# Kernel tuning notes

Measured on AMD Instinct MI355X. Metric: run time of the kernel, lower is better.

## Reference

```python
import jax, jax.numpy as jnp
import numpy as np

Q_BITS = 4
Q_MAX = 2 ** (Q_BITS - 1) - 1  # 7 for 4-bit symmetric

B, S, D_IN, D_OUT = 4, 2048, 4096, 11008


def setup_inputs() -> dict:
    key = jax.random.key(0)
    kx, kw = jax.random.split(key)
    x = jax.random.normal(kx, (B, S, D_IN), dtype=jnp.float32)
    weight = jax.random.normal(kw, (D_OUT, D_IN), dtype=jnp.float32)
    bias = jnp.zeros((1, D_OUT), dtype=jnp.float32)
    return {"x": x, "weight": weight, "bias": bias}


def _quant_act_per_token_absmax(t):
    # t: [N, D]; symmetric fake-quant with per-token (per-row) absmax scale
    scales = jnp.max(jnp.abs(t), axis=-1, keepdims=True)
    scales = jnp.maximum(scales, 1e-5) / Q_MAX
    return jnp.round(t / scales) * scales


def reference(x, weight, bias):
    x_shape = x.shape
    xf = x.reshape(-1, x_shape[-1])          # [B*S, D_in]
    q_x = _quant_act_per_token_absmax(xf)    # fake-quantized activations
    y = q_x @ weight.T + bias                # [B*S, D_out]
    return y.reshape(x_shape[0], x_shape[1], -1)
```

## Files before the change

kernel.cpp:

```cpp
#include <hip/hip_runtime.h>
#include <hip/hip_bf16.h>

#define M_DIM 8192
#define N_DIM 11008
#define K_DIM 4096
#define NT 32
#define RROW ((size_t)64 * K_DIM)

typedef __attribute__((ext_vector_type(4))) int i32x4;

__global__ void quant_x_kernel(const float* __restrict__ x,
                               char* __restrict__ xq, float* __restrict__ sx) {
  const int row = blockIdx.x;
  const int t = threadIdx.x;
  const float4* xr4 = (const float4*)(x + (size_t)row * K_DIM);
  float4 v[4];
  float amax = 0.0f;
#pragma unroll
  for (int i = 0; i < 4; ++i) {
    v[i] = xr4[t + 256 * i];
    amax = fmaxf(amax, fmaxf(fmaxf(fabsf(v[i].x), fabsf(v[i].y)),
                             fmaxf(fabsf(v[i].z), fabsf(v[i].w))));
  }
#pragma unroll
  for (int off = 32; off > 0; off >>= 1)
    amax = fmaxf(amax, __shfl_xor(amax, off, 64));
  __shared__ float red[4];
  if ((t & 63) == 0) red[t >> 6] = amax;
  __syncthreads();
  amax = fmaxf(fmaxf(red[0], red[1]), fmaxf(red[2], red[3]));
  const float s = fmaxf(amax, 1e-5f) / 7.0f;
  if (t == 0) sx[row] = s;
  char q[16];
#pragma unroll
  for (int i = 0; i < 4; ++i) {
    q[i * 4 + 0] = (char)(int)rintf(v[i].x / s);
    q[i * 4 + 1] = (char)(int)rintf(v[i].y / s);
    q[i * 4 + 2] = (char)(int)rintf(v[i].z / s);
    q[i * 4 + 3] = (char)(int)rintf(v[i].w / s);
  }
  *(int4*)(xq + (size_t)row * K_DIM + t * 16) = *(int4*)q;
}

__global__ void quant_w_kernel(const float* __restrict__ w,
                               char* __restrict__ wq, float* __restrict__ sw) {
  const int row = blockIdx.x;
  const int t = threadIdx.x;
  const float4* wr4 = (const float4*)(w + (size_t)row * K_DIM);
  float4 v[4];
  float amax = 0.0f;
#pragma unroll
  for (int i = 0; i < 4; ++i) {
    v[i] = wr4[t + 256 * i];
    amax = fmaxf(amax, fmaxf(fmaxf(fabsf(v[i].x), fabsf(v[i].y)),
                             fmaxf(fabsf(v[i].z), fabsf(v[i].w))));
  }
#pragma unroll
  for (int off = 32; off > 0; off >>= 1)
    amax = fmaxf(amax, __shfl_xor(amax, off, 64));
  __shared__ float red[4];
  if ((t & 63) == 0) red[t >> 6] = amax;
  __syncthreads();
  amax = fmaxf(fmaxf(red[0], red[1]), fmaxf(red[2], red[3]));
  const float s = fmaxf(amax, 1e-30f) / 127.0f;
  if (t == 0) sw[row] = s;
  char q[16];
#pragma unroll
  for (int i = 0; i < 4; ++i) {
    q[i * 4 + 0] = (char)(int)rintf(v[i].x / s);
    q[i * 4 + 1] = (char)(int)rintf(v[i].y / s);
    q[i * 4 + 2] = (char)(int)rintf(v[i].z / s);
    q[i * 4 + 3] = (char)(int)rintf(v[i].w / s);
  }
  *(int4*)(wq + (size_t)row * K_DIM + t * 16) = *(int4*)q;
}

#define GL(g, d)                                                             \
  __builtin_amdgcn_global_load_lds(                                          \
      (const __attribute__((address_space(1))) void*)(g),                    \
      (__attribute__((address_space(3))) void*)(d), 16, 0, 0)

template<bool STG>
__device__ __forceinline__ void tile_body(const char* paRow, const char* pbRow, int colswz,
    const char* gAn, const char* gBn, char* dA, char* dB, i32x4 (&acc)[8][4]) {
  if constexpr (STG) {
    GL(gAn, dA);                    GL(gAn + 2 * RROW, dA + 16384);
    GL(gBn, dB);                    GL(gBn + RROW, dB + 8192);
    GL(gBn + 2 * RROW, dB + 16384); GL(gBn + 3 * RROW, dB + 24576);
    GL(gAn + RROW, dA + 8192);      GL(gAn + 3 * RROW, dA + 24576);
  }
  const int c0 = colswz;
  const int c1 = colswz ^ 64;
  i32x4 a0[4], a1[4], a2[4], a3[4], b0[4], b1[4];
#pragma unroll
  for (int i = 0; i < 4; ++i) a0[i] = *(const i32x4*)(paRow + i * 2048 + c0);
#pragma unroll
  for (int i = 0; i < 4; ++i) b0[i] = *(const i32x4*)(pbRow + i * 2048 + c0);
#pragma unroll
  for (int i = 0; i < 4; ++i) a1[i] = *(const i32x4*)(paRow + 8192 + i * 2048 + c0);
#pragma unroll
  for (int m = 0; m < 4; ++m)
#pragma unroll
    for (int n = 0; n < 4; ++n)
      acc[m][n] = __builtin_amdgcn_mfma_i32_16x16x64_i8(a0[m], b0[n], acc[m][n], 0, 0, 0);
#pragma unroll
  for (int i = 0; i < 4; ++i) a2[i] = *(const i32x4*)(paRow + i * 2048 + c1);
#pragma unroll
  for (int i = 0; i < 4; ++i) b1[i] = *(const i32x4*)(pbRow + i * 2048 + c1);
#pragma unroll
  for (int m = 0; m < 4; ++m)
#pragma unroll
    for (int n = 0; n < 4; ++n)
      acc[4 + m][n] = __builtin_amdgcn_mfma_i32_16x16x64_i8(a1[m], b0[n], acc[4 + m][n], 0, 0, 0);
#pragma unroll
  for (int i = 0; i < 4; ++i) a3[i] = *(const i32x4*)(paRow + 8192 + i * 2048 + c1);
#pragma unroll
  for (int m = 0; m < 4; ++m)
#pragma unroll
    for (int n = 0; n < 4; ++n)
      acc[m][n] = __builtin_amdgcn_mfma_i32_16x16x64_i8(a2[m], b1[n], acc[m][n], 0, 0, 0);
#pragma unroll
  for (int m = 0; m < 4; ++m)
#pragma unroll
    for (int n = 0; n < 4; ++n)
      acc[4 + m][n] = __builtin_amdgcn_mfma_i32_16x16x64_i8(a3[m], b1[n], acc[4 + m][n], 0, 0, 0);
}

__global__ __launch_bounds__(512, 2) void gemm_kernel(
    const char* __restrict__ xq, const char* __restrict__ wq,
    const float* __restrict__ sx, const float* __restrict__ sw,
    const float* __restrict__ bias, float* __restrict__ out) {
  __shared__ char lds_c[131072];

  const int tid = threadIdx.x;
  const int lane = tid & 63;
  const int wave = tid >> 6;
  const int wm = wave >> 2;
  const int wn = wave & 3;
  const int lr = lane & 15;

  const int bid = blockIdx.x;
  const int sw_id = (bid & 7) * 172 + (bid >> 3);
  const int bm = sw_id / 43, bn = sw_id % 43;
  const int m0 = bm * 256, n0 = bn * 256;

  const int srow = tid >> 3;
  const int srccb = ((tid & 7) << 4) ^ ((srow & 7) << 4);
  const char* gA0 = xq + (size_t)(m0 + srow) * K_DIM + srccb;
  const char* gB0 = wq + (size_t)(n0 + srow) * K_DIM + srccb;
  char* dA0 = lds_c + wave * 1024;
  char* dB0 = lds_c + 65536 + wave * 1024;

  const int aRowOff = (wm * 128 + lr) * 128;
  const int bRowOff = (wn * 64 + lr) * 128;
  const int colswz = ((lane >> 4) << 4) ^ ((lr & 7) << 4);

  i32x4 acc[8][4] = {};

  GL(gA0, dA0);                    GL(gA0 + 2 * RROW, dA0 + 16384);
  GL(gB0, dB0);                    GL(gB0 + RROW, dB0 + 8192);
  GL(gB0 + 2 * RROW, dB0 + 16384); GL(gB0 + 3 * RROW, dB0 + 24576);
  GL(gA0 + RROW, dA0 + 8192);      GL(gA0 + 3 * RROW, dA0 + 24576);
  __syncthreads();

  for (int t = 0; t < NT - 1; ++t) {
    const int buf = t & 1;
    tile_body<true>(lds_c + buf * 32768 + aRowOff,
                    lds_c + 65536 + buf * 32768 + bRowOff, colswz,
                    gA0 + (size_t)(t + 1) * 128, gB0 + (size_t)(t + 1) * 128,
                    dA0 + (1 - buf) * 32768, dB0 + (1 - buf) * 32768, acc);
    __syncthreads();
  }
  tile_body<false>(lds_c + ((NT - 1) & 1) * 32768 + aRowOff,
                   lds_c + 65536 + ((NT - 1) & 1) * 32768 + bRowOff, colswz,
                   nullptr, nullptr, nullptr, nullptr, acc);

  const int orow0 = m0 + wm * 128 + (lane >> 4) * 4;
  const int ocol0 = n0 + wn * 64 + lr;
  float bv[4], swv[4];
#pragma unroll
  for (int fc = 0; fc < 4; ++fc) {
    bv[fc] = bias[ocol0 + fc * 16];
    swv[fc] = sw[ocol0 + fc * 16];
  }
#pragma unroll
  for (int fr = 0; fr < 8; ++fr) {
#pragma unroll
    for (int j = 0; j < 4; ++j) {
      const int grow = orow0 + fr * 16 + j;
      const float s = sx[grow];
      float* op = out + (size_t)grow * N_DIM + ocol0;
#pragma unroll
      for (int fc = 0; fc < 4; ++fc)
        op[fc * 16] = (float)acc[fr][fc][j] * (s * swv[fc]) + bv[fc];
    }
  }
}

extern "C" void kernel_launch(void* const* d_in, const int* in_sizes, int n_in,
                              void* d_out, int out_size, void* d_ws, size_t ws_size,
                              hipStream_t stream) {
  (void)in_sizes; (void)n_in; (void)out_size; (void)ws_size;
  const float* x = (const float*)d_in[0];
  const float* w = (const float*)d_in[1];
  const float* bias = (const float*)d_in[2];
  float* out = (float*)d_out;

  char* ws = (char*)d_ws;
  float* sx = (float*)ws;
  float* sw = (float*)(ws + 32768);
  char* xq8 = ws + 131072;
  char* wq8 = ws + 131072 + (size_t)M_DIM * K_DIM;

  quant_x_kernel<<<M_DIM, 256, 0, stream>>>(x, xq8, sx);
  quant_w_kernel<<<N_DIM, 256, 0, stream>>>(w, wq8, sw);
  gemm_kernel<<<dim3((M_DIM / 256) * (N_DIM / 256)), 512, 0, stream>>>(xq8, wq8, sx, sw, bias, out);
}
```

Measured before the change: 452.2 us.

## Software-pipeline MFMA groups across K tiles with sched barriers

Restructures the GEMM main loop so the last MFMA group of each K tile is deferred into the next tile. There it overlaps with the LDS reads issued after the barrier, and the barrier moves to the start of each tile. Sched barriers pin the interleaving of LDS reads and MFMA groups, so matrix work is always pending while fragments load. This costs extra registers for the carried fragments, which may pressure occupancy at 2 blocks of 512 threads.

```diff
diff --git a/kernel.cpp b/kernel.cpp
--- a/kernel.cpp
+++ b/kernel.cpp
@@ -80,50 +80,56 @@
       (const __attribute__((address_space(1))) void*)(g),                    \
       (__attribute__((address_space(3))) void*)(d), 16, 0, 0)
 
-template<bool STG>
-__device__ __forceinline__ void tile_body(const char* paRow, const char* pbRow, int colswz,
-    const char* gAn, const char* gBn, char* dA, char* dB, i32x4 (&acc)[8][4]) {
+template<int KK>
+__device__ __forceinline__ void read_g1(const char* paRow, const char* pbRow, int colswz,
+                                        i32x4 (&a)[4], i32x4 (&b)[4]) {
+  const int c = colswz ^ (KK * 64);
+#pragma unroll
+  for (int i = 0; i < 4; ++i) a[i] = *(const i32x4*)(paRow + i * 2048 + c);
+#pragma unroll
+  for (int i = 0; i < 4; ++i) b[i] = *(const i32x4*)(pbRow + i * 2048 + c);
+}
+template<int KK>
+__device__ __forceinline__ void read_g2(const char* paRow, int colswz, i32x4 (&a)[4]) {
+  const int c = colswz ^ (KK * 64);
+#pragma unroll
+  for (int i = 0; i < 4; ++i) a[i] = *(const i32x4*)(paRow + 8192 + i * 2048 + c);
+}
+template<int OFF>
+__device__ __forceinline__ void mfma16(const i32x4 (&a)[4], const i32x4 (&b)[4],
+                                       i32x4 (&acc)[8][4]) {
+#pragma unroll
+  for (int m = 0; m < 4; ++m)
+#pragma unroll
+    for (int n = 0; n < 4; ++n)
+      acc[OFF + m][n] = __builtin_amdgcn_mfma_i32_16x16x64_i8(a[m], b[n], acc[OFF + m][n], 0, 0, 0);
+}
+
+template<bool FIRST, bool STG>
+__device__ __forceinline__ void tile(const char* paRow, const char* pbRow, int colswz,
+    const char* gAn, const char* gBn, char* dA, char* dB,
+    i32x4 (&acc)[8][4], i32x4 (&bP)[4], i32x4 (&a2P)[4]) {
+  __syncthreads();
   if constexpr (STG) {
     GL(gAn, dA);                    GL(gAn + 2 * RROW, dA + 16384);
     GL(gBn, dB);                    GL(gBn + RROW, dB + 8192);
     GL(gBn + 2 * RROW, dB + 16384); GL(gBn + 3 * RROW, dB + 24576);
     GL(gAn + RROW, dA + 8192);      GL(gAn + 3 * RROW, dA + 24576);
   }
-  const int c0 = colswz;
-  const int c1 = colswz ^ 64;
-  i32x4 a0[4], a1[4], a2[4], a3[4], b0[4], b1[4];
-#pragma unroll
-  for (int i = 0; i < 4; ++i) a0[i] = *(const i32x4*)(paRow + i * 2048 + c0);
-#pragma unroll
-  for (int i = 0; i < 4; ++i) b0[i] = *(const i32x4*)(pbRow + i * 2048 + c0);
-#pragma unroll
-  for (int i = 0; i < 4; ++i) a1[i] = *(const i32x4*)(paRow + 8192 + i * 2048 + c0);
-#pragma unroll
-  for (int m = 0; m < 4; ++m)
-#pragma unroll
-    for (int n = 0; n < 4; ++n)
-      acc[m][n] = __builtin_amdgcn_mfma_i32_16x16x64_i8(a0[m], b0[n], acc[m][n], 0, 0, 0);
-#pragma unroll
-  for (int i = 0; i < 4; ++i) a2[i] = *(const i32x4*)(paRow + i * 2048 + c1);
-#pragma unroll
-  for (int i = 0; i < 4; ++i) b1[i] = *(const i32x4*)(pbRow + i * 2048 + c1);
-#pragma unroll
-  for (int m = 0; m < 4; ++m)
-#pragma unroll
-    for (int n = 0; n < 4; ++n)
-      acc[4 + m][n] = __builtin_amdgcn_mfma_i32_16x16x64_i8(a1[m], b0[n], acc[4 + m][n], 0, 0, 0);
-#pragma unroll
-  for (int i = 0; i < 4; ++i) a3[i] = *(const i32x4*)(paRow + 8192 + i * 2048 + c1);
-#pragma unroll
-  for (int m = 0; m < 4; ++m)
-#pragma unroll
-    for (int n = 0; n < 4; ++n)
-      acc[m][n] = __builtin_amdgcn_mfma_i32_16x16x64_i8(a2[m], b1[n], acc[m][n], 0, 0, 0);
-#pragma unroll
-  for (int m = 0; m < 4; ++m)
-#pragma unroll
-    for (int n = 0; n < 4; ++n)
-      acc[4 + m][n] = __builtin_amdgcn_mfma_i32_16x16x64_i8(a3[m], b1[n], acc[4 + m][n], 0, 0, 0);
+  i32x4 a10[4], b0[4], a20[4], a11[4], b1[4], a21[4];
+  read_g1<0>(paRow, pbRow, colswz, a10, b0);
+  if constexpr (!FIRST) mfma16<4>(a2P, bP, acc);
+  __builtin_amdgcn_sched_barrier(0);
+  read_g2<0>(paRow, colswz, a20);
+  mfma16<0>(a10, b0, acc);
+  __builtin_amdgcn_sched_barrier(0);
+  read_g1<1>(paRow, pbRow, colswz, a11, b1);
+  mfma16<4>(a20, b0, acc);
+  __builtin_amdgcn_sched_barrier(0);
+  read_g2<1>(paRow, colswz, a21);
+  mfma16<0>(a11, b1, acc);
+#pragma unroll
+  for (int i = 0; i < 4; ++i) { bP[i] = b1[i]; a2P[i] = a21[i]; }
 }
 
 __global__ __launch_bounds__(512, 2) void gemm_kernel(
@@ -156,24 +162,26 @@
   const int colswz = ((lane >> 4) << 4) ^ ((lr & 7) << 4);
 
   i32x4 acc[8][4] = {};
+  i32x4 bP[4], a2P[4];
 
   GL(gA0, dA0);                    GL(gA0 + 2 * RROW, dA0 + 16384);
   GL(gB0, dB0);                    GL(gB0 + RROW, dB0 + 8192);
   GL(gB0 + 2 * RROW, dB0 + 16384); GL(gB0 + 3 * RROW, dB0 + 24576);
   GL(gA0 + RROW, dA0 + 8192);      GL(gA0 + 3 * RROW, dA0 + 24576);
-  __syncthreads();
-
-  for (int t = 0; t < NT - 1; ++t) {
+
+  tile<true, true>(lds_c + aRowOff, lds_c + 65536 + bRowOff, colswz,
+                   gA0 + 128, gB0 + 128, dA0 + 32768, dB0 + 32768, acc, bP, a2P);
+  for (int t = 1; t < NT - 1; ++t) {
     const int buf = t & 1;
-    tile_body<true>(lds_c + buf * 32768 + aRowOff,
-                    lds_c + 65536 + buf * 32768 + bRowOff, colswz,
-                    gA0 + (size_t)(t + 1) * 128, gB0 + (size_t)(t + 1) * 128,
-                    dA0 + (1 - buf) * 32768, dB0 + (1 - buf) * 32768, acc);
-    __syncthreads();
-  }
-  tile_body<false>(lds_c + ((NT - 1) & 1) * 32768 + aRowOff,
-                   lds_c + 65536 + ((NT - 1) & 1) * 32768 + bRowOff, colswz,
-                   nullptr, nullptr, nullptr, nullptr, acc);
+    tile<false, true>(lds_c + buf * 32768 + aRowOff,
+                      lds_c + 65536 + buf * 32768 + bRowOff, colswz,
+                      gA0 + (size_t)(t + 1) * 128, gB0 + (size_t)(t + 1) * 128,
+                      dA0 + (1 - buf) * 32768, dB0 + (1 - buf) * 32768, acc, bP, a2P);
+  }
+  tile<false, false>(lds_c + ((NT - 1) & 1) * 32768 + aRowOff,
+                     lds_c + 65536 + ((NT - 1) & 1) * 32768 + bRowOff, colswz,
+                     nullptr, nullptr, nullptr, nullptr, acc, bP, a2P);
+  mfma16<4>(a2P, bP, acc);
 
   const int orow0 = m0 + wm * 128 + (lane >> 4) * 4;
   const int ocol0 = n0 + wn * 64 + lr;
```

New measurement: 436.3 us. -3.5%, faster.

## Load B fragments directly from global into registers, stage only A in LDS

Applied to the files above, without the earlier changes.

The GEMM no longer stages the weight tile through LDS. Each wave loads its B fragments straight from global memory into registers, prefetching the next half-K slice during the MFMA work, while A stays double-buffered in LDS. This halves LDS usage and removes B's LDS write/read traffic, and the block index mapping changes to a column-major tile order. In exchange each B row is fetched once per wave (wm duplicates) instead of once per block, and the code depends on register prefetch latency hiding; N=11008 is not a multiple of 256, so the bn tail handling should be checked.

```diff
diff --git a/kernel.cpp b/kernel.cpp
--- a/kernel.cpp
+++ b/kernel.cpp
@@ -80,57 +80,50 @@
       (const __attribute__((address_space(1))) void*)(g),                    \
       (__attribute__((address_space(3))) void*)(d), 16, 0, 0)
 
-template<bool STG>
-__device__ __forceinline__ void tile_body(const char* paRow, const char* pbRow, int colswz,
-    const char* gAn, const char* gBn, char* dA, char* dB, i32x4 (&acc)[8][4]) {
+#define MFMA_I8 __builtin_amdgcn_mfma_i32_16x16x64_i8
+
+template<bool STG, bool PB>
+__device__ __forceinline__ void tile(const char* pa, int colswz,
+    const char* gAn, char* dA, const char* gBt,
+    i32x4 (&bk0)[4], i32x4 (&bk1)[4], i32x4 (&acc)[8][4]) {
+  __syncthreads();
   if constexpr (STG) {
-    GL(gAn, dA);                    GL(gAn + 2 * RROW, dA + 16384);
-    GL(gBn, dB);                    GL(gBn + RROW, dB + 8192);
-    GL(gBn + 2 * RROW, dB + 16384); GL(gBn + 3 * RROW, dB + 24576);
-    GL(gAn + RROW, dA + 8192);      GL(gAn + 3 * RROW, dA + 24576);
-  }
-  const int c0 = colswz;
-  const int c1 = colswz ^ 64;
-  i32x4 a0[4], a1[4], a2[4], a3[4], b0[4], b1[4];
-#pragma unroll
-  for (int i = 0; i < 4; ++i) a0[i] = *(const i32x4*)(paRow + i * 2048 + c0);
-#pragma unroll
-  for (int i = 0; i < 4; ++i) b0[i] = *(const i32x4*)(pbRow + i * 2048 + c0);
-#pragma unroll
-  for (int i = 0; i < 4; ++i) a1[i] = *(const i32x4*)(paRow + 8192 + i * 2048 + c0);
-#pragma unroll
-  for (int m = 0; m < 4; ++m)
+    GL(gAn, dA);                GL(gAn + RROW, dA + 8192);
+    GL(gAn + 2 * RROW, dA + 16384); GL(gAn + 3 * RROW, dA + 24576);
+  }
+#pragma unroll
+  for (int f = 0; f < 4; ++f)
+    bk1[f] = *(const i32x4*)(gBt + 64 + (size_t)f * 16 * K_DIM);
+  i32x4 a[8];
+#pragma unroll
+  for (int f = 0; f < 8; ++f)
+    a[f] = *(const i32x4*)(pa + f * 2048 + colswz);
+#pragma unroll
+  for (int m = 0; m < 8; ++m)
 #pragma unroll
     for (int n = 0; n < 4; ++n)
-      acc[m][n] = __builtin_amdgcn_mfma_i32_16x16x64_i8(a0[m], b0[n], acc[m][n], 0, 0, 0);
-#pragma unroll
-  for (int i = 0; i < 4; ++i) a2[i] = *(const i32x4*)(paRow + i * 2048 + c1);
-#pragma unroll
-  for (int i = 0; i < 4; ++i) b1[i] = *(const i32x4*)(pbRow + i * 2048 + c1);
-#pragma unroll
-  for (int m = 0; m < 4; ++m)
+      acc[m][n] = MFMA_I8(a[m], bk0[n], acc[m][n], 0, 0, 0);
+  __builtin_amdgcn_sched_barrier(0);
+  if constexpr (PB) {
+#pragma unroll
+    for (int f = 0; f < 4; ++f)
+      bk0[f] = *(const i32x4*)(gBt + 128 + (size_t)f * 16 * K_DIM);
+  }
+#pragma unroll
+  for (int f = 0; f < 8; ++f)
+    a[f] = *(const i32x4*)(pa + f * 2048 + (colswz ^ 64));
+#pragma unroll
+  for (int m = 0; m < 8; ++m)
 #pragma unroll
     for (int n = 0; n < 4; ++n)
-      acc[4 + m][n] = __builtin_amdgcn_mfma_i32_16x16x64_i8(a1[m], b0[n], acc[4 + m][n], 0, 0, 0);
-#pragma unroll
-  for (int i = 0; i < 4; ++i) a3[i] = *(const i32x4*)(paRow + 8192 + i * 2048 + c1);
-#pragma unroll
-  for (int m = 0; m < 4; ++m)
-#pragma unroll
-    for (int n = 0; n < 4; ++n)
-      acc[m][n] = __builtin_amdgcn_mfma_i32_16x16x64_i8(a2[m], b1[n], acc[m][n], 0, 0, 0);
-#pragma unroll
-  for (int m = 0; m < 4; ++m)
-#pragma unroll
-    for (int n = 0; n < 4; ++n)
-      acc[4 + m][n] = __builtin_amdgcn_mfma_i32_16x16x64_i8(a3[m], b1[n], acc[4 + m][n], 0, 0, 0);
+      acc[m][n] = MFMA_I8(a[m], bk1[n], acc[m][n], 0, 0, 0);
 }
 
 __global__ __launch_bounds__(512, 2) void gemm_kernel(
     const char* __restrict__ xq, const char* __restrict__ wq,
     const float* __restrict__ sx, const float* __restrict__ sw,
     const float* __restrict__ bias, float* __restrict__ out) {
-  __shared__ char lds_c[131072];
+  __shared__ char lds_c[65536];
 
   const int tid = threadIdx.x;
   const int lane = tid & 63;
@@ -141,39 +134,36 @@
 
   const int bid = blockIdx.x;
   const int sw_id = (bid & 7) * 172 + (bid >> 3);
-  const int bm = sw_id / 43, bn = sw_id % 43;
+  const int bm = sw_id & 31, bn = sw_id >> 5;
   const int m0 = bm * 256, n0 = bn * 256;
 
   const int srow = tid >> 3;
   const int srccb = ((tid & 7) << 4) ^ ((srow & 7) << 4);
   const char* gA0 = xq + (size_t)(m0 + srow) * K_DIM + srccb;
-  const char* gB0 = wq + (size_t)(n0 + srow) * K_DIM + srccb;
   char* dA0 = lds_c + wave * 1024;
-  char* dB0 = lds_c + 65536 + wave * 1024;
 
   const int aRowOff = (wm * 128 + lr) * 128;
-  const int bRowOff = (wn * 64 + lr) * 128;
   const int colswz = ((lane >> 4) << 4) ^ ((lr & 7) << 4);
 
+  const char* gB0 = wq + (size_t)(n0 + wn * 64 + lr) * K_DIM + ((lane >> 4) << 4);
+
   i32x4 acc[8][4] = {};
-
-  GL(gA0, dA0);                    GL(gA0 + 2 * RROW, dA0 + 16384);
-  GL(gB0, dB0);                    GL(gB0 + RROW, dB0 + 8192);
-  GL(gB0 + 2 * RROW, dB0 + 16384); GL(gB0 + 3 * RROW, dB0 + 24576);
-  GL(gA0 + RROW, dA0 + 8192);      GL(gA0 + 3 * RROW, dA0 + 24576);
-  __syncthreads();
+  i32x4 bk0[4], bk1[4];
+
+  GL(gA0, dA0);                GL(gA0 + RROW, dA0 + 8192);
+  GL(gA0 + 2 * RROW, dA0 + 16384); GL(gA0 + 3 * RROW, dA0 + 24576);
+#pragma unroll
+  for (int f = 0; f < 4; ++f)
+    bk0[f] = *(const i32x4*)(gB0 + (size_t)f * 16 * K_DIM);
 
   for (int t = 0; t < NT - 1; ++t) {
     const int buf = t & 1;
-    tile_body<true>(lds_c + buf * 32768 + aRowOff,
-                    lds_c + 65536 + buf * 32768 + bRowOff, colswz,
-                    gA0 + (size_t)(t + 1) * 128, gB0 + (size_t)(t + 1) * 128,
-                    dA0 + (1 - buf) * 32768, dB0 + (1 - buf) * 32768, acc);
-    __syncthreads();
-  }
-  tile_body<false>(lds_c + ((NT - 1) & 1) * 32768 + aRowOff,
-                   lds_c + 65536 + ((NT - 1) & 1) * 32768 + bRowOff, colswz,
-                   nullptr, nullptr, nullptr, nullptr, acc);
+    tile<true, true>(lds_c + buf * 32768 + aRowOff, colswz,
+                     gA0 + (size_t)(t + 1) * 128, dA0 + (1 - buf) * 32768,
+                     gB0 + (size_t)t * 128, bk0, bk1, acc);
+  }
+  tile<false, false>(lds_c + ((NT - 1) & 1) * 32768 + aRowOff, colswz,
+                     nullptr, nullptr, gB0 + (size_t)(NT - 1) * 128, bk0, bk1, acc);
 
   const int orow0 = m0 + wm * 128 + (lane >> 4) * 4;
   const int ocol0 = n0 + wn * 64 + lr;
```

After: 632.5 us. 39.9% more time.
